# Optimization experiments

Measured on AMD Instinct MI355X. Metric: run time of the kernel, lower is better.

## Reference

```python
import jax, jax.numpy as jnp
import numpy as np

N_NODES = 50000
N_EDGES = 800000
IN_DIM, HID, OUT = 128, 256, 256
N_GRAPHS = 256
EPS = 1e-5


def _gcn_conv(x, W, b, src, dst, n):
    # PyG GCNConv: h = x @ W; propagate with sym-norm over A + I; add bias.
    h = x @ W  # (N, F)
    deg = jax.ops.segment_sum(jnp.ones((src.shape[0],), x.dtype), dst, num_segments=n) + 1.0
    dis = jax.lax.rsqrt(deg)  # D^{-1/2} of A+I
    norm = dis[src] * dis[dst]  # per-edge weight
    agg = jax.ops.segment_sum(h[src] * norm[:, None], dst, num_segments=n)
    agg = agg + h * (dis * dis)[:, None]  # self-loop contribution
    return agg + b


def _layer_norm(x, g, b):
    mu = jnp.mean(x, axis=-1, keepdims=True)
    var = jnp.mean((x - mu) ** 2, axis=-1, keepdims=True)
    return (x - mu) * jax.lax.rsqrt(var + EPS) * g + b


def setup_inputs() -> dict:
    key = jax.random.key(0)
    ks = jax.random.split(key, 8)
    x = jax.random.normal(ks[0], (N_NODES, IN_DIM), jnp.float32)
    W1 = jax.random.normal(ks[1], (IN_DIM, HID), jnp.float32) * (1.0 / np.sqrt(IN_DIM))
    W2 = jax.random.normal(ks[2], (HID, HID), jnp.float32) * (1.0 / np.sqrt(HID))
    W3 = jax.random.normal(ks[3], (HID, OUT), jnp.float32) * (1.0 / np.sqrt(HID))
    edge_index = jax.random.randint(ks[4], (2, N_EDGES), 0, N_NODES, dtype=jnp.int64)
    batch = jnp.sort(jax.random.randint(ks[5], (N_NODES,), 0, N_GRAPHS, dtype=jnp.int64))
    return {
        "x": x,
        "W1": W1, "b1": jnp.zeros((HID,), jnp.float32),
        "g1": jnp.ones((HID,), jnp.float32), "be1": jnp.zeros((HID,), jnp.float32),
        "W2": W2, "b2": jnp.zeros((HID,), jnp.float32),
        "g2": jnp.ones((HID,), jnp.float32), "be2": jnp.zeros((HID,), jnp.float32),
        "W3": W3, "b3": jnp.zeros((OUT,), jnp.float32),
        "edge_index": edge_index,
        "batch": batch,
        "num_graphs": N_GRAPHS,
    }


def reference(x, W1, b1, g1, be1, W2, b2, g2, be2, W3, b3, edge_index, batch, num_graphs):
    n = x.shape[0]
    src, dst = edge_index[0], edge_index[1]
    h = _gcn_conv(x, W1, b1, src, dst, n)
    h = _layer_norm(jax.nn.relu(h), g1, be1)  # dropout = identity (eval)
    h = _gcn_conv(h, W2, b2, src, dst, n)
    h = _layer_norm(jax.nn.relu(h), g2, be2)
    h = _gcn_conv(h, W3, b3, src, dst, n)
    # segment mean pool per graph
    sums = jax.ops.segment_sum(h, batch, num_segments=num_graphs)
    cnts = jax.ops.segment_sum(jnp.ones((n,), h.dtype), batch, num_segments=num_graphs)
    return sums / cnts[:, None]
```

## Files before the change

kernel.cpp:

```cpp
#include <hip/hip_runtime.h>

#define N_NODES 50000
#define MROWS   50048
#define N_EDGES 800000
#define IN_DIM  128
#define HID     256
#define NGRAPH  256
#define LN_EPS  1e-5f

typedef __attribute__((ext_vector_type(8))) short bf16x8;
typedef __attribute__((ext_vector_type(4))) float f32x4;
typedef __attribute__((ext_vector_type(4))) unsigned int u32x4;

#define NCHUNK  128
#define CHUNK   6250
#define HWORDS  12500

#define PAD_E (N_EDGES + 7 * N_NODES)

#define W_DEG      0
#define W_FLAG     (W_DEG + N_NODES)
#define W_BSUM     (W_FLAG + 16)
#define W_BPRE     (W_BSUM + 256)
#define W_GOFF     (W_BPRE + 256)
#define W_OFFS     (W_GOFF + NGRAPH + 8)
#define W_DIS      (W_OFFS + N_NODES + 8)
#define W_CSR      (((W_DIS + N_NODES) + 3) & ~3)
#define W_WT       (W_CSR + 2 * PAD_E)
#define W_ZH       (((W_WT + 163840) + 3) & ~3)
#define W_ZL       (W_ZH + (MROWS * HID / 2))
#define W_H        (W_ZL + (MROWS * HID / 2))

#define WT1H 0
#define WT1L 32768
#define WT2H 65536
#define WT2L 131072
#define WT3H 196608
#define WT3L 262144

__device__ __forceinline__ unsigned short f2b(float f) {
    unsigned int u = __float_as_uint(f);
    unsigned int r = (u + 0x7FFFu + ((u >> 16) & 1u)) >> 16;
    return (unsigned short)r;
}
__device__ __forceinline__ float b2f(unsigned short h) {
    return __uint_as_float(((unsigned int)h) << 16);
}
__device__ __forceinline__ f32x4 cvt4(uint2 u) {
    f32x4 r;
    r[0] = __uint_as_float(u.x << 16);
    r[1] = __uint_as_float(u.x & 0xffff0000u);
    r[2] = __uint_as_float(u.y << 16);
    r[3] = __uint_as_float(u.y & 0xffff0000u);
    return r;
}

__global__ __launch_bounds__(256) void zero_kernel(unsigned int* __restrict__ p, int n) {
    int i = blockIdx.x * 256 + threadIdx.x;
    if (i < n) p[i] = 0u;
}

__global__ __launch_bounds__(256) void detect_kernel(const unsigned int* __restrict__ ei,
                                                     int* __restrict__ flag) {
    int e = blockIdx.x * 256 + threadIdx.x;
    if (e >= N_EDGES) return;
    if (ei[2 * e + 1] != 0u) *flag = 1;
}

__global__ __launch_bounds__(256) void hist_kernel(const void* __restrict__ ei,
                                                   const int* __restrict__ flag,
                                                   unsigned int* __restrict__ partial) {
    __shared__ unsigned int h[HWORDS];
    int c = blockIdx.x >> 1, hf = blockIdx.x & 1;
    int t = threadIdx.x;
    for (int i = t; i < HWORDS; i += 256) h[i] = 0u;
    __syncthreads();
    bool is32 = (*flag != 0);
    int e0 = c * CHUNK;
    for (int k = 0; k < 25; ++k) {
        int e = e0 + t + k * 256;
        if (e < e0 + CHUNK) {
            int d = is32 ? ((const int*)ei)[N_EDGES + e]
                         : (int)((const long long*)ei)[N_EDGES + e];
            if (((d >= 25000) ? 1 : 0) == hf) {
                int w = (d - hf * 25000) >> 1;
                atomicAdd(&h[w], (d & 1) ? 0x10000u : 1u);
            }
        }
    }
    __syncthreads();
    unsigned int* dst = partial + (size_t)blockIdx.x * HWORDS;
    for (int i = t; i < HWORDS; i += 256) dst[i] = h[i];
}

__global__ __launch_bounds__(256) void merge_kernel(unsigned int* __restrict__ partial,
                                                    int* __restrict__ deg) {
    int w = blockIdx.x * 256 + threadIdx.x;
    if (w >= 25000) return;
    int hf = (w >= HWORDS) ? 1 : 0;
    int wi = w - hf * HWORDS;
    unsigned int run_lo = 0, run_hi = 0;
    for (int c = 0; c < NCHUNK; ++c) {
        size_t idx = ((size_t)(c * 2 + hf)) * HWORDS + wi;
        unsigned int u = partial[idx];
        partial[idx] = run_lo | (run_hi << 16);
        run_lo += u & 0xffffu;
        run_hi += u >> 16;
    }
    deg[2 * w]     = (int)run_lo;
    deg[2 * w + 1] = (int)run_hi;
}

__global__ __launch_bounds__(256) void blocksum_kernel(const int* __restrict__ deg,
                                                       int* __restrict__ bsum) {
    int b = blockIdx.x, t = threadIdx.x;
    int i = b * 256 + t;
    int pd = (i < N_NODES) ? ((deg[i] + 7) & ~7) : 0;
    int lane = t & 63, w = t >> 6;
    int s = pd;
    #pragma unroll
    for (int o = 32; o >= 1; o >>= 1) s += __shfl_xor(s, o, 64);
    __shared__ int ws[4];
    if (lane == 0) ws[w] = s;
    __syncthreads();
    if (t == 0) bsum[b] = ws[0] + ws[1] + ws[2] + ws[3];
}

__global__ __launch_bounds__(256) void scanb_kernel(const int* __restrict__ bsum,
                                                    int* __restrict__ bpre) {
    int t = threadIdx.x;
    int lane = t & 63, w = t >> 6;
    int x = (t < 196) ? bsum[t] : 0;
    int inc = x;
    #pragma unroll
    for (int o = 1; o < 64; o <<= 1) {
        int u = __shfl_up(inc, o, 64);
        if (lane >= o) inc += u;
    }
    __shared__ int wsA[4];
    if (lane == 63) wsA[w] = inc;
    __syncthreads();
    int base = 0;
    for (int k = 0; k < w; ++k) base += wsA[k];
    bpre[t] = base + inc - x;
}

__global__ __launch_bounds__(256) void finalize_kernel(const int* __restrict__ deg,
                                                       const int* __restrict__ bpre,
                                                       int* __restrict__ offs,
                                                       float* __restrict__ dis) {
    int b = blockIdx.x, t = threadIdx.x;
    int i = b * 256 + t;
    int d = (i < N_NODES) ? deg[i] : 0;
    int pd = (d + 7) & ~7;
    int lane = t & 63, w = t >> 6;
    int inc = pd;
    #pragma unroll
    for (int o = 1; o < 64; o <<= 1) {
        int u = __shfl_up(inc, o, 64);
        if (lane >= o) inc += u;
    }
    __shared__ int ws[4];
    if (lane == 63) ws[w] = inc;
    __syncthreads();
    int base = 0;
    for (int k = 0; k < w; ++k) base += ws[k];
    int pre = base + inc - pd;
    if (i < N_NODES) {
        offs[i] = bpre[b] + pre;
        dis[i] = rsqrtf((float)d + 1.0f);
    }
    if (i == N_NODES - 1) offs[N_NODES] = bpre[b] + pre + pd;
}

__global__ __launch_bounds__(256) void scatter2_kernel(const void* __restrict__ ei,
                                                       const int* __restrict__ flag,
                                                       const int* __restrict__ offs,
                                                       const float* __restrict__ dis,
                                                       const unsigned int* __restrict__ partial,
                                                       int2* __restrict__ csr) {
    __shared__ unsigned int cur[HWORDS];
    int c = blockIdx.x >> 1, hf = blockIdx.x & 1;
    int t = threadIdx.x;
    for (int i = t; i < HWORDS; i += 256) cur[i] = 0u;
    __syncthreads();
    bool is32 = (*flag != 0);
    const unsigned int* rel = partial + (size_t)blockIdx.x * HWORDS;
    int e0 = c * CHUNK;
    for (int k = 0; k < 25; ++k) {
        int e = e0 + t + k * 256;
        if (e < e0 + CHUNK) {
            int s, d;
            if (is32) {
                const int* p = (const int*)ei;
                s = p[e]; d = p[N_EDGES + e];
            } else {
                const long long* p = (const long long*)ei;
                s = (int)p[e]; d = (int)p[N_EDGES + e];
            }
            if (((d >= 25000) ? 1 : 0) == hf) {
                int w = (d - hf * 25000) >> 1;
                unsigned int old = atomicAdd(&cur[w], (d & 1) ? 0x10000u : 1u);
                unsigned int p0 = (d & 1) ? (old >> 16) : (old & 0xffffu);
                unsigned int rp = rel[w];
                unsigned int r = (d & 1) ? (rp >> 16) : (rp & 0xffffu);
                int pos = offs[d] + (int)r + (int)p0;
                int2 rec;
                rec.x = s << 9;
                rec.y = __float_as_int(dis[s] * dis[d]);
                csr[pos] = rec;
            }
        }
    }
}

__global__ __launch_bounds__(256) void goffs_kernel(const void* __restrict__ bt,
                                                    const int* __restrict__ flag,
                                                    int* __restrict__ goffs) {
    int v = blockIdx.x * 256 + threadIdx.x;
    if (v >= N_NODES) return;
    bool is32 = (*flag != 0);
    int b = is32 ? ((const int*)bt)[v] : (int)((const long long*)bt)[v];
    if (v == 0) {
        for (int g = 0; g <= b; ++g) goffs[g] = 0;
    } else {
        int pb = is32 ? ((const int*)bt)[v - 1] : (int)((const long long*)bt)[v - 1];
        for (int g = pb + 1; g <= b; ++g) goffs[g] = v;
    }
    if (v == N_NODES - 1) {
        for (int g = b + 1; g <= NGRAPH; ++g) goffs[g] = N_NODES;
    }
}

#define XSPLIT_BLOCKS 6250
__global__ __launch_bounds__(256) void prep_w(const float* __restrict__ x,
                                              const float* __restrict__ W1,
                                              const float* __restrict__ W2,
                                              const float* __restrict__ W3,
                                              unsigned short* __restrict__ xh,
                                              unsigned short* __restrict__ wt) {
    int b = blockIdx.x;
    int t = threadIdx.x;
    if (b < XSPLIT_BLOCKS) {
        int i = b * 256 + t;
        float4 v = ((const float4*)x)[i];
        ushort4 h;
        h.x = f2b(v.x); h.y = f2b(v.y); h.z = f2b(v.z); h.w = f2b(v.w);
        ((ushort4*)xh)[i] = h;
    } else {
        int wb = b - XSPLIT_BLOCKS;
        const float* W; int K, k, bh, bl;
        if (wb < 128)      { W = W1; K = 128; k = wb;       bh = WT1H; bl = WT1L; }
        else if (wb < 384) { W = W2; K = 256; k = wb - 128; bh = WT2H; bl = WT2L; }
        else               { W = W3; K = 256; k = wb - 384; bh = WT3H; bl = WT3L; }
        int n = t;
        float val = W[k * HID + n];
        unsigned short hv = f2b(val);
        unsigned short lv = f2b(val - b2f(hv));
        wt[bh + n * K + k] = hv;
        wt[bl + n * K + k] = lv;
    }
}

__global__ __launch_bounds__(256) void gemm_bf16(const unsigned short* __restrict__ A,
                                                 const unsigned short* __restrict__ Bh,
                                                 const unsigned short* __restrict__ Bl,
                                                 unsigned short* __restrict__ C,
                                                 int K) {
    __shared__ char lds[3 * 128 * 80];
    int tid = threadIdx.x;
    int bm = blockIdx.x * 128;
    int bn = blockIdx.y * 128;
    int lane = tid & 63, wid = tid >> 6;
    int wm = wid >> 1, wn = wid & 1;
    int lr = lane & 15, lc = lane >> 4;
    f32x4 acc[4][4];
    #pragma unroll
    for (int i = 0; i < 4; ++i)
        #pragma unroll
        for (int j = 0; j < 4; ++j)
            acc[i][j] = (f32x4){0.f, 0.f, 0.f, 0.f};

    for (int k0 = 0; k0 < K; k0 += 32) {
        #pragma unroll
        for (int c8 = 0; c8 < 6; ++c8) {
            const int tile = c8 >> 1;
            const unsigned short* __restrict__ src =
                (tile == 0) ? A : (tile == 1) ? Bh : Bl;
            int c = ((c8 & 1) << 8) + tid;
            int rr = c >> 2, q = c & 3;
            int row = ((tile == 0) ? bm : bn) + rr;
            u32x4 v = *(const u32x4*)(src + (size_t)row * K + k0 + q * 8);
            *(u32x4*)(lds + tile * 10240 + rr * 80 + q * 16) = v;
        }
        __syncthreads();
        bf16x8 af[4], bh[4], bl[4];
        #pragma unroll
        for (int f = 0; f < 4; ++f) {
            af[f] = *(const bf16x8*)(lds +             (wm * 64 + f * 16 + lr) * 80 + lc * 16);
            bh[f] = *(const bf16x8*)(lds + 10240     + (wn * 64 + f * 16 + lr) * 80 + lc * 16);
            bl[f] = *(const bf16x8*)(lds + 2 * 10240 + (wn * 64 + f * 16 + lr) * 80 + lc * 16);
        }
        #pragma unroll
        for (int fi = 0; fi < 4; ++fi) {
            #pragma unroll
            for (int fj = 0; fj < 4; ++fj) {
                acc[fi][fj] = __builtin_amdgcn_mfma_f32_16x16x32_bf16(af[fi], bh[fj], acc[fi][fj], 0, 0, 0);
                acc[fi][fj] = __builtin_amdgcn_mfma_f32_16x16x32_bf16(af[fi], bl[fj], acc[fi][fj], 0, 0, 0);
            }
        }
        __syncthreads();
    }
    #pragma unroll
    for (int fi = 0; fi < 4; ++fi) {
        int rbase = bm + wm * 64 + fi * 16 + lc * 4;
        #pragma unroll
        for (int fj = 0; fj < 4; ++fj) {
            int col = bn + wn * 64 + fj * 16 + lr;
            #pragma unroll
            for (int r = 0; r < 4; ++r) {
                C[(size_t)(rbase + r) * HID + col] = f2b(acc[fi][fj][r]);
            }
        }
    }
}

#define DECL_CH(P) int4 P##c0, P##c1, P##c2, P##c3; \
                   uint2 P##h0, P##h1, P##h2, P##h3, P##h4, P##h5, P##h6, P##h7;

#define LOAD8(P, idx) do { \
    const int4* _q = (const int4*)(csr + (idx)); \
    P##c0 = _q[0]; P##c1 = _q[1]; P##c2 = _q[2]; P##c3 = _q[3]; \
    P##h0 = *(const uint2*)(Hl + P##c0.x); \
    P##h1 = *(const uint2*)(Hl + P##c0.z); \
    P##h2 = *(const uint2*)(Hl + P##c1.x); \
    P##h3 = *(const uint2*)(Hl + P##c1.z); \
    P##h4 = *(const uint2*)(Hl + P##c2.x); \
    P##h5 = *(const uint2*)(Hl + P##c2.z); \
    P##h6 = *(const uint2*)(Hl + P##c3.x); \
    P##h7 = *(const uint2*)(Hl + P##c3.z); \
} while (0)

#define FMA4U(hv, wv, a) do { a += cvt4(hv) * (wv); } while (0)

#define CONS8(P, a) do { \
    FMA4U(P##h0, __int_as_float(P##c0.y), a); \
    FMA4U(P##h1, __int_as_float(P##c0.w), a); \
    FMA4U(P##h2, __int_as_float(P##c1.y), a); \
    FMA4U(P##h3, __int_as_float(P##c1.w), a); \
    FMA4U(P##h4, __int_as_float(P##c2.y), a); \
    FMA4U(P##h5, __int_as_float(P##c2.w), a); \
    FMA4U(P##h6, __int_as_float(P##c3.y), a); \
    FMA4U(P##h7, __int_as_float(P##c3.w), a); \
} while (0)

template <int MODE>
__global__ __launch_bounds__(256) void agg_kernel(const unsigned short* __restrict__ H,
                                                  const float* __restrict__ dis,
                                                  const int* __restrict__ offs,
                                                  const int2* __restrict__ csr,
                                                  const float* __restrict__ bias,
                                                  const float* __restrict__ gamma,
                                                  const float* __restrict__ beta,
                                                  unsigned short* __restrict__ Z,
                                                  float* __restrict__ O) {
    int v = blockIdx.x * 4 + (threadIdx.x >> 6);
    int l = threadIdx.x & 63;
    const char* Hl = (const char*)H + l * 8;

    float dv = dis[v];
    uint2 a0u = ((const uint2*)(H + (size_t)v * HID))[l];
    f32x4 acc = cvt4(a0u) * (dv * dv);

    int i = offs[v];
    int n = (offs[v + 1] - i) >> 3;
    DECL_CH(A)
    DECL_CH(B)
    if (n > 0) LOAD8(A, i);
    if (n > 1) LOAD8(B, i + 8);
    int c = 0;
    while (c + 2 < n) {
        if ((c & 1) == 0) { CONS8(A, acc); LOAD8(A, i + 16); }
        else              { CONS8(B, acc); LOAD8(B, i + 16); }
        i += 8; ++c;
    }
    if (c < n) {
        if ((c & 1) == 0) CONS8(A, acc); else CONS8(B, acc);
        ++c;
    }
    if (c < n) {
        if ((c & 1) == 0) CONS8(A, acc); else CONS8(B, acc);
    }

    f32x4 b4 = *(const f32x4*)(bias + l * 4);
    if (MODE == 0) {
        acc += b4;
        acc[0] = fmaxf(acc[0], 0.f); acc[1] = fmaxf(acc[1], 0.f);
        acc[2] = fmaxf(acc[2], 0.f); acc[3] = fmaxf(acc[3], 0.f);
        float s = acc[0] + acc[1] + acc[2] + acc[3];
        #pragma unroll
        for (int o = 32; o >= 1; o >>= 1) s += __shfl_xor(s, o, 64);
        float mu = s * (1.0f / HID);
        f32x4 d = acc - mu;
        float vs = d[0] * d[0] + d[1] * d[1] + d[2] * d[2] + d[3] * d[3];
        #pragma unroll
        for (int o = 32; o >= 1; o >>= 1) vs += __shfl_xor(vs, o, 64);
        float inv = rsqrtf(vs * (1.0f / HID) + LN_EPS);
        f32x4 g4 = *(const f32x4*)(gamma + l * 4);
        f32x4 be4 = *(const f32x4*)(beta + l * 4);
        ushort4 zh;
        zh.x = f2b(d[0] * inv * g4[0] + be4[0]);
        zh.y = f2b(d[1] * inv * g4[1] + be4[1]);
        zh.z = f2b(d[2] * inv * g4[2] + be4[2]);
        zh.w = f2b(d[3] * inv * g4[3] + be4[3]);
        *(ushort4*)(Z + (size_t)v * HID + l * 4) = zh;
    } else {
        acc += b4;
        *(f32x4*)(O + (size_t)v * HID + l * 4) = acc;
    }
}

__global__ __launch_bounds__(256) void pool_kernel(const float* __restrict__ O,
                                                   const int* __restrict__ goffs,
                                                   float* __restrict__ out) {
    int g = blockIdx.x, t = threadIdx.x;
    int l = t & 63, w = t >> 6;
    int s = goffs[g], e = goffs[g + 1];
    float4 acc = make_float4(0.f, 0.f, 0.f, 0.f);
    for (int v = s + w; v < e; v += 4) {
        float4 r = ((const float4*)(O + (size_t)v * HID))[l];
        acc.x += r.x; acc.y += r.y; acc.z += r.z; acc.w += r.w;
    }
    __shared__ float4 red[4][64];
    red[w][l] = acc;
    __syncthreads();
    if (w == 0) {
        float4 r0 = red[0][l], r1 = red[1][l], r2 = red[2][l], r3 = red[3][l];
        float inv = 1.0f / (float)(e - s);
        float4 o;
        o.x = (r0.x + r1.x + r2.x + r3.x) * inv;
        o.y = (r0.y + r1.y + r2.y + r3.y) * inv;
        o.z = (r0.z + r1.z + r2.z + r3.z) * inv;
        o.w = (r0.w + r1.w + r2.w + r3.w) * inv;
        ((float4*)(out + (size_t)g * HID))[l] = o;
    }
}

extern "C" void kernel_launch(void* const* d_in, const int* in_sizes, int n_in,
                              void* d_out, int out_size, void* d_ws, size_t ws_size,
                              hipStream_t stream) {
    const float* x   = (const float*)d_in[0];
    const float* W1  = (const float*)d_in[1];
    const float* b1  = (const float*)d_in[2];
    const float* g1  = (const float*)d_in[3];
    const float* be1 = (const float*)d_in[4];
    const float* W2  = (const float*)d_in[5];
    const float* b2  = (const float*)d_in[6];
    const float* g2  = (const float*)d_in[7];
    const float* be2 = (const float*)d_in[8];
    const float* W3  = (const float*)d_in[9];
    const float* b3  = (const float*)d_in[10];
    const void*  ei  = d_in[11];
    const void*  bt  = d_in[12];
    float* out = (float*)d_out;

    unsigned int* ws = (unsigned int*)d_ws;
    int*   deg    = (int*)(ws + W_DEG);
    int*   flag   = (int*)(ws + W_FLAG);
    int*   bsum   = (int*)(ws + W_BSUM);
    int*   bpre   = (int*)(ws + W_BPRE);
    int*   goffs  = (int*)(ws + W_GOFF);
    int*   offs   = (int*)(ws + W_OFFS);
    float* dis    = (float*)(ws + W_DIS);
    int2*  csr    = (int2*)(ws + W_CSR);
    unsigned short* wt = (unsigned short*)(ws + W_WT);
    unsigned short* Zbuf = (unsigned short*)(ws + W_ZH);
    unsigned short* xh = Zbuf;
    unsigned short* Hbuf = (unsigned short*)(ws + W_H);
    unsigned int*   partial = (unsigned int*)(ws + W_H);
    float* Obuf = (float*)(ws + W_ZH);

    const int EB = (N_EDGES + 255) / 256;
    const int NB = (N_NODES + 255) / 256;

    zero_kernel<<<1, 256, 0, stream>>>(ws + W_FLAG, 16);
    zero_kernel<<<(2 * PAD_E + 255) / 256, 256, 0, stream>>>(ws + W_CSR, 2 * PAD_E);
    detect_kernel<<<EB, 256, 0, stream>>>((const unsigned int*)ei, flag);
    hist_kernel<<<2 * NCHUNK, 256, 0, stream>>>(ei, flag, partial);
    merge_kernel<<<(25000 + 255) / 256, 256, 0, stream>>>(partial, deg);
    blocksum_kernel<<<NB, 256, 0, stream>>>(deg, bsum);
    scanb_kernel<<<1, 256, 0, stream>>>(bsum, bpre);
    finalize_kernel<<<NB, 256, 0, stream>>>(deg, bpre, offs, dis);
    scatter2_kernel<<<2 * NCHUNK, 256, 0, stream>>>(ei, flag, offs, dis, partial, csr);
    goffs_kernel<<<NB, 256, 0, stream>>>(bt, flag, goffs);
    prep_w<<<XSPLIT_BLOCKS + 640, 256, 0, stream>>>(x, W1, W2, W3, xh, wt);

    dim3 gg(MROWS / 128, HID / 128);
    const int AB = N_NODES / 4;

    gemm_bf16<<<gg, 256, 0, stream>>>(xh, wt + WT1H, wt + WT1L, Hbuf, IN_DIM);
    agg_kernel<0><<<AB, 256, 0, stream>>>(Hbuf, dis, offs, csr, b1, g1, be1, Zbuf, nullptr);
    gemm_bf16<<<gg, 256, 0, stream>>>(Zbuf, wt + WT2H, wt + WT2L, Hbuf, HID);
    agg_kernel<0><<<AB, 256, 0, stream>>>(Hbuf, dis, offs, csr, b2, g2, be2, Zbuf, nullptr);
    gemm_bf16<<<gg, 256, 0, stream>>>(Zbuf, wt + WT3H, wt + WT3L, Hbuf, HID);
    agg_kernel<1><<<AB, 256, 0, stream>>>(Hbuf, dis, offs, csr, b3, nullptr, nullptr, nullptr, Obuf);
    pool_kernel<<<NGRAPH, 256, 0, stream>>>(Obuf, goffs, out);
}
```

Measured before the change: 403.3 us.

## Pad CSR rows to multiples of 4 and zero only padding slots

Each node's CSR row is now padded to a multiple of 4 instead of 8, which cuts the number of zero-weight padding edges the three aggregation passes must gather. The full CSR memset is replaced by a small kernel that zeroes only the padding slots. The aggregation loop now uses three rotating 4-edge buffers, keeping about the same number of loads in flight. The tail handling is more complex and the padzero kernel adds one launch.

```diff
diff --git a/kernel.cpp b/kernel.cpp
--- a/kernel.cpp
+++ b/kernel.cpp
@@ -16,7 +16,7 @@
 #define CHUNK   6250
 #define HWORDS  12500
 
-#define PAD_E (N_EDGES + 7 * N_NODES)
+#define PAD_E (N_EDGES + 3 * N_NODES)
 
 #define W_DEG      0
 #define W_FLAG     (W_DEG + N_NODES)
@@ -115,7 +115,7 @@
                                                        int* __restrict__ bsum) {
     int b = blockIdx.x, t = threadIdx.x;
     int i = b * 256 + t;
-    int pd = (i < N_NODES) ? ((deg[i] + 7) & ~7) : 0;
+    int pd = (i < N_NODES) ? ((deg[i] + 3) & ~3) : 0;
     int lane = t & 63, w = t >> 6;
     int s = pd;
     #pragma unroll
@@ -152,7 +152,7 @@
     int b = blockIdx.x, t = threadIdx.x;
     int i = b * 256 + t;
     int d = (i < N_NODES) ? deg[i] : 0;
-    int pd = (d + 7) & ~7;
+    int pd = (d + 3) & ~3;
     int lane = t & 63, w = t >> 6;
     int inc = pd;
     #pragma unroll
@@ -171,6 +171,18 @@
         dis[i] = rsqrtf((float)d + 1.0f);
     }
     if (i == N_NODES - 1) offs[N_NODES] = bpre[b] + pre + pd;
+}
+
+__global__ __launch_bounds__(256) void padzero_kernel(const int* __restrict__ deg,
+                                                      const int* __restrict__ offs,
+                                                      int2* __restrict__ csr) {
+    int v = blockIdx.x * 256 + threadIdx.x;
+    if (v >= N_NODES) return;
+    int d = deg[v];
+    int e = offs[v] + d;
+    int pe = offs[v] + ((d + 3) & ~3);
+    int2 z; z.x = 0; z.y = 0;
+    for (; e < pe; ++e) csr[e] = z;
 }
 
 __global__ __launch_bounds__(256) void scatter2_kernel(const void* __restrict__ ei,
@@ -325,33 +337,24 @@
     }
 }
 
-#define DECL_CH(P) int4 P##c0, P##c1, P##c2, P##c3; \
-                   uint2 P##h0, P##h1, P##h2, P##h3, P##h4, P##h5, P##h6, P##h7;
-
-#define LOAD8(P, idx) do { \
+#define DECL_C4(P) int4 P##c0, P##c1; uint2 P##h0, P##h1, P##h2, P##h3;
+
+#define LOAD4(P, idx) do { \
     const int4* _q = (const int4*)(csr + (idx)); \
-    P##c0 = _q[0]; P##c1 = _q[1]; P##c2 = _q[2]; P##c3 = _q[3]; \
+    P##c0 = _q[0]; P##c1 = _q[1]; \
     P##h0 = *(const uint2*)(Hl + P##c0.x); \
     P##h1 = *(const uint2*)(Hl + P##c0.z); \
     P##h2 = *(const uint2*)(Hl + P##c1.x); \
     P##h3 = *(const uint2*)(Hl + P##c1.z); \
-    P##h4 = *(const uint2*)(Hl + P##c2.x); \
-    P##h5 = *(const uint2*)(Hl + P##c2.z); \
-    P##h6 = *(const uint2*)(Hl + P##c3.x); \
-    P##h7 = *(const uint2*)(Hl + P##c3.z); \
 } while (0)
 
 #define FMA4U(hv, wv, a) do { a += cvt4(hv) * (wv); } while (0)
 
-#define CONS8(P, a) do { \
+#define CONS4(P, a) do { \
     FMA4U(P##h0, __int_as_float(P##c0.y), a); \
     FMA4U(P##h1, __int_as_float(P##c0.w), a); \
     FMA4U(P##h2, __int_as_float(P##c1.y), a); \
     FMA4U(P##h3, __int_as_float(P##c1.w), a); \
-    FMA4U(P##h4, __int_as_float(P##c2.y), a); \
-    FMA4U(P##h5, __int_as_float(P##c2.w), a); \
-    FMA4U(P##h6, __int_as_float(P##c3.y), a); \
-    FMA4U(P##h7, __int_as_float(P##c3.w), a); \
 } while (0)
 
 template <int MODE>
@@ -373,24 +376,26 @@
     f32x4 acc = cvt4(a0u) * (dv * dv);
 
     int i = offs[v];
-    int n = (offs[v + 1] - i) >> 3;
-    DECL_CH(A)
-    DECL_CH(B)
-    if (n > 0) LOAD8(A, i);
-    if (n > 1) LOAD8(B, i + 8);
+    int n = (offs[v + 1] - i) >> 2;
+    DECL_C4(A)
+    DECL_C4(B)
+    DECL_C4(C)
+    if (n > 0) LOAD4(A, i);
+    if (n > 1) LOAD4(B, i + 4);
+    if (n > 2) LOAD4(C, i + 8);
     int c = 0;
-    while (c + 2 < n) {
-        if ((c & 1) == 0) { CONS8(A, acc); LOAD8(A, i + 16); }
-        else              { CONS8(B, acc); LOAD8(B, i + 16); }
-        i += 8; ++c;
-    }
-    if (c < n) {
-        if ((c & 1) == 0) CONS8(A, acc); else CONS8(B, acc);
-        ++c;
-    }
-    if (c < n) {
-        if ((c & 1) == 0) CONS8(A, acc); else CONS8(B, acc);
-    }
+    while (c + 6 <= n) {
+        CONS4(A, acc); LOAD4(A, i + 12);
+        CONS4(B, acc); LOAD4(B, i + 16);
+        CONS4(C, acc); LOAD4(C, i + 20);
+        i += 12; c += 3;
+    }
+    int r = n - c;
+    if (r >= 1) { CONS4(A, acc); if (r >= 4) LOAD4(A, i + 12); }
+    if (r >= 2) { CONS4(B, acc); if (r >= 5) LOAD4(B, i + 16); }
+    if (r >= 3) CONS4(C, acc);
+    if (r >= 4) CONS4(A, acc);
+    if (r >= 5) CONS4(B, acc);
 
     f32x4 b4 = *(const f32x4*)(bias + l * 4);
     if (MODE == 0) {
@@ -484,13 +489,13 @@
     const int NB = (N_NODES + 255) / 256;
 
     zero_kernel<<<1, 256, 0, stream>>>(ws + W_FLAG, 16);
-    zero_kernel<<<(2 * PAD_E + 255) / 256, 256, 0, stream>>>(ws + W_CSR, 2 * PAD_E);
     detect_kernel<<<EB, 256, 0, stream>>>((const unsigned int*)ei, flag);
     hist_kernel<<<2 * NCHUNK, 256, 0, stream>>>(ei, flag, partial);
     merge_kernel<<<(25000 + 255) / 256, 256, 0, stream>>>(partial, deg);
     blocksum_kernel<<<NB, 256, 0, stream>>>(deg, bsum);
     scanb_kernel<<<1, 256, 0, stream>>>(bsum, bpre);
     finalize_kernel<<<NB, 256, 0, stream>>>(deg, bpre, offs, dis);
+    padzero_kernel<<<NB, 256, 0, stream>>>(deg, offs, csr);
     scatter2_kernel<<<2 * NCHUNK, 256, 0, stream>>>(ei, flag, offs, dis, partial, csr);
     goffs_kernel<<<NB, 256, 0, stream>>>(bt, flag, goffs);
     prep_w<<<XSPLIT_BLOCKS + 640, 256, 0, stream>>>(x, W1, W2, W3, xh, wt);
```

Result: faster. 384.5 us (-4.7%).
